# Performance work log

Measured on AMD Instinct MI355X. Metric: run time of the kernel, lower is better.

## Reference

```python
import jax, jax.numpy as jnp
import numpy as np

EPS = 1e-5
K = 16  # neighbors

def bn(x, g, b):
    # BatchNorm in training mode: stats over all axes except the last (channel)
    ax = tuple(range(x.ndim - 1))
    m = x.mean(ax, keepdims=True)
    v = x.var(ax, keepdims=True)
    return g * (x - m) * jax.lax.rsqrt(v + EPS) + b

def setup_inputs() -> dict:
    key = jax.random.key(0)
    ks = jax.random.split(key, 12)
    B, N, M, C, D = 2, 16384, 4096, 32, 64
    H = D // 2
    p = lambda k, s: jax.random.normal(k, s, dtype=jnp.float32) * 0.1
    inp = {}
    inp["xyz"] = jax.random.normal(ks[0], (B, N, 3), dtype=jnp.float32)
    inp["feats"] = jax.random.normal(ks[1], (B, C, N), dtype=jnp.float32)
    inp["sample_idx"] = jax.random.randint(ks[2], (B, M), 0, N, dtype=jnp.int32)
    # RelativePosEncoder mlp: Conv2d(10, H, 1) + BN
    inp["W_pos"] = p(ks[3], (10, H)); inp["b_pos"] = jnp.zeros(H); inp["g_pos"] = jnp.ones(H); inp["be_pos"] = jnp.zeros(H)
    # feature_mlp: Conv2d(C, H, 1) + BN
    inp["W_feat"] = p(ks[4], (C, H)); inp["b_feat"] = jnp.zeros(H); inp["g_feat"] = jnp.ones(H); inp["be_feat"] = jnp.zeros(H)
    # attention score mlp: Conv2d(D, D, 1, bias=False)
    inp["W_score"] = p(ks[5], (D, D))
    # out_mlp: Conv1d(D, D, 1, bias=False) + BN
    inp["W_out"] = p(ks[6], (D, D)); inp["g_out"] = jnp.ones(D); inp["be_out"] = jnp.zeros(D)
    # LFA shortcut: Conv1d(C, D, 1, bias=False) + BN
    inp["W_sc1"] = p(ks[7], (C, D)); inp["g_sc1"] = jnp.ones(D); inp["be_sc1"] = jnp.zeros(D)
    # unit shortcut: Conv1d(C, D, 1, bias=False) + BN
    inp["W_sc2"] = p(ks[8], (C, D)); inp["g_sc2"] = jnp.ones(D); inp["be_sc2"] = jnp.zeros(D)
    return inp

def reference(xyz, feats, sample_idx,
              W_pos, b_pos, g_pos, be_pos,
              W_feat, b_feat, g_feat, be_feat,
              W_score,
              W_out, g_out, be_out,
              W_sc1, g_sc1, be_sc1,
              W_sc2, g_sc2, be_sc2):
    B, C, N = feats.shape
    featsT = jnp.transpose(feats, (0, 2, 1))                    # [B,N,C]
    xyz_ds = jnp.take_along_axis(xyz, sample_idx[:, :, None], axis=1)  # [B,M,3]
    # KNN: squared distances are monotone in cdist -> same topk indices
    d2 = jnp.sum((xyz_ds[:, :, None, :] - xyz[:, None, :, :]) ** 2, axis=-1)  # [B,M,N]
    _, knn_idx = jax.lax.top_k(-d2, K)                           # [B,M,K]
    gather = jax.vmap(lambda pts, idx: pts[idx])
    neigh_xyz = gather(xyz, knn_idx)                             # [B,M,K,3]
    neigh_feats = gather(featsT, knn_idx)                        # [B,M,K,C]
    center_feats = jnp.take_along_axis(featsT, sample_idx[:, :, None], axis=1)  # [B,M,C]
    # relative position encoding
    center = jnp.broadcast_to(xyz_ds[:, :, None, :], neigh_xyz.shape)
    rel = xyz_ds[:, :, None, :] - neigh_xyz                      # [B,M,K,3]
    dist = jnp.linalg.norm(rel, axis=-1, keepdims=True)          # [B,M,K,1]
    posf = jnp.concatenate([center, neigh_xyz, rel, dist], axis=-1)  # [B,M,K,10]
    pos_feats = jax.nn.relu(bn(posf @ W_pos + b_pos, g_pos, be_pos))       # [B,M,K,H]
    feat_feats = jax.nn.relu(bn(neigh_feats @ W_feat + b_feat, g_feat, be_feat))  # [B,M,K,H]
    combined = jnp.concatenate([feat_feats, pos_feats], axis=-1)  # [B,M,K,D]
    # attention pooling: softmax over the K (neighbor) axis
    scores = jax.nn.softmax(combined @ W_score, axis=2)
    pooled = jnp.sum(scores * combined, axis=2)                  # [B,M,D]
    out = jax.nn.relu(bn(pooled @ W_out, g_out, be_out))         # [B,M,D]
    sc1 = bn(jnp.mean(neigh_feats, axis=2) @ W_sc1, g_sc1, be_sc1)
    f_lfa = out + sc1
    f_sc = bn(center_feats @ W_sc2, g_sc2, be_sc2)
    y = jax.nn.relu(f_lfa + f_sc)                                # [B,M,D]
    return xyz_ds, jnp.transpose(y, (0, 2, 1)), sample_idx
```

## Files before the change

kernel.cpp:

```cpp
#include <hip/hip_runtime.h>
#include <math.h>

#define BB 2
#define NN 16384
#define MM 4096
#define C_IN 32
#define D_DIM 64
#define H_DIM 32
#define KNB 16
#define EPSV 1e-5f
#define FLT_BIG 3.0e38f
#define CAPK 128
#define NSPL 4
#define SPTS (NN / NSPL)

#define SPOS_SUM 0
#define SPOS_SQ 32
#define SFEAT_SUM 64
#define SFEAT_SQ 96
#define SSC1_SUM 128
#define SSC1_SQ 192
#define SSC2_SUM 256
#define SSC2_SQ 320
#define SOUT_SUM 384
#define SOUT_SQ 448
#define STATS_LEN 512
#define PA_W 384
#define PB_W 128
#define NBLK (BB * MM / 4)

typedef float f32x2 __attribute__((ext_vector_type(2)));

__device__ __forceinline__ f32x2 mk2_r24(float a, float b) {
    f32x2 r; r.x = a; r.y = b; return r;
}

__device__ __forceinline__ int clampi_r24(int v, int lo, int hi) {
    return v < lo ? lo : (v > hi ? hi : v);
}

__global__ __launch_bounds__(256) void prep_r24(const float* __restrict__ feats,
                                                const float* __restrict__ xyz,
                                                const int* __restrict__ sample_idx,
                                                float* __restrict__ featsT,
                                                float* __restrict__ xyz4,
                                                float* __restrict__ stats,
                                                float* __restrict__ out) {
    __shared__ float tile[C_IN][65];
    const int tid = threadIdx.x;
    const int b = blockIdx.x >> 8;
    const int n0 = (blockIdx.x & 255) * 64;
#pragma unroll
    for (int it = 0; it < 8; ++it) {
        int c = (tid >> 6) + 4 * it;
        int n = tid & 63;
        tile[c][n] = feats[((size_t)b * C_IN + c) * NN + n0 + n];
    }
    int e = blockIdx.x * 256 + tid;
    if (e < STATS_LEN) stats[e] = 0.f;
    if (e < BB * NN) {
        float x = xyz[e * 3 + 0], y = xyz[e * 3 + 1], z = xyz[e * 3 + 2];
        xyz4[e * 4 + 0] = x;
        xyz4[e * 4 + 1] = y;
        xyz4[e * 4 + 2] = z;
        xyz4[e * 4 + 3] = x * x + y * y + z * z;
    }
    if (e < BB * MM) {
        int bb2 = e >> 12;
        int sidx = clampi_r24(sample_idx[e], 0, NN - 1);
        const float* p = xyz + (size_t)(bb2 * NN + sidx) * 3;
        out[e * 3 + 0] = p[0];
        out[e * 3 + 1] = p[1];
        out[e * 3 + 2] = p[2];
        out[BB * MM * 3 + BB * D_DIM * MM + e] = (float)sample_idx[e];
    }
    __syncthreads();
#pragma unroll
    for (int it = 0; it < 8; ++it) {
        int c = tid & 31;
        int nn = (tid >> 5) + 8 * it;
        featsT[((size_t)b * NN + n0 + nn) * C_IN + c] = tile[c][nn];
    }
}

__device__ void knn_fullsplit_r24(const float* __restrict__ base4, int n0,
                                  float m2x, float m2y, float m2z, int lane,
                                  float* __restrict__ outd, int* __restrict__ outi) {
    float d2v[KNB]; int iv[KNB];
#pragma unroll
    for (int i = 0; i < KNB; i++) { d2v[i] = FLT_BIG; iv[i] = 0x7FFFFFFF; }
    float curmax = FLT_BIG; int amax = 0;
    for (int t = 0; t < SPTS / 64; ++t) {
        int n = n0 + lane + t * 64;
        const float4 p = *reinterpret_cast<const float4*>(base4 + (size_t)n * 4);
        float d2 = fmaf(p.x, m2x, p.w);
        d2 = fmaf(p.y, m2y, d2);
        d2 = fmaf(p.z, m2z, d2);
        if (d2 < curmax) {
#pragma unroll
            for (int i = 0; i < KNB; i++)
                if (i == amax) { d2v[i] = d2; iv[i] = n; }
            curmax = d2v[0]; amax = 0;
#pragma unroll
            for (int i = 1; i < KNB; i++)
                if (d2v[i] > curmax) { curmax = d2v[i]; amax = i; }
        }
    }
#pragma unroll
    for (int i = 0; i < KNB; i++) {
#pragma unroll
        for (int j = 0; j < KNB - 1; j++) {
            bool sw = (d2v[j] > d2v[j + 1]) ||
                      (d2v[j] == d2v[j + 1] && iv[j] > iv[j + 1]);
            if (sw) {
                float td = d2v[j]; d2v[j] = d2v[j + 1]; d2v[j + 1] = td;
                int   ti = iv[j];  iv[j]  = iv[j + 1];  iv[j + 1]  = ti;
            }
        }
    }
    float myd = FLT_BIG; int myidx = 0x7FFFFFFF;
#pragma unroll 1
    for (int r = 0; r < KNB; r++) {
        float cv = d2v[0]; int cid = iv[0]; int ml = lane;
#pragma unroll
        for (int off = 32; off > 0; off >>= 1) {
            float ov = __shfl_xor(cv, off);
            int   oid = __shfl_xor(cid, off);
            int   ol = __shfl_xor(ml, off);
            bool take = (ov < cv) || (ov == cv && oid < cid);
            cv = take ? ov : cv; cid = take ? oid : cid; ml = take ? ol : ml;
        }
        if (lane == r) { myd = cv; myidx = cid; }
        if (lane == ml) {
#pragma unroll
            for (int i = 0; i < KNB - 1; i++) { d2v[i] = d2v[i + 1]; iv[i] = iv[i + 1]; }
            d2v[KNB - 1] = FLT_BIG; iv[KNB - 1] = 0x7FFFFFFF;
        }
    }
    if (lane < KNB) { outd[lane] = myd; outi[lane] = myidx; }
}

__global__ __launch_bounds__(256) void knn_r24(const float* __restrict__ xyz4,
                                               const int* __restrict__ sample_idx,
                                               float* __restrict__ cand_d,
                                               int* __restrict__ cand_i) {
    __shared__ float bufd[32][CAPK];
    __shared__ int   bufi[32][CAPK];
    const int tid = threadIdx.x;
    const int w = tid >> 6, lane = tid & 63;
    const int split = blockIdx.x & (NSPL - 1);
    const int qgrp = blockIdx.x >> 2;
    const int qbase = qgrp * 32 + w * 8;
    const int b = qbase >> 12;
    const int n0 = split * SPTS;
    const float* base4 = xyz4 + (size_t)b * NN * 4;
    const float4* p4 = reinterpret_cast<const float4*>(base4) + n0 + lane;

    float m2x[8], m2y[8], m2z[8], md[8], v16[8];
#pragma unroll
    for (int j = 0; j < 8; j++) {
        int s = clampi_r24(sample_idx[qbase + j], 0, NN - 1);
        m2x[j] = -2.f * base4[(size_t)s * 4 + 0];
        m2y[j] = -2.f * base4[(size_t)s * 4 + 1];
        m2z[j] = -2.f * base4[(size_t)s * 4 + 2];
        md[j] = FLT_BIG;
    }
#pragma unroll 4
    for (int it = 0; it < SPTS / 64; ++it) {
        const float4 p = p4[(size_t)it * 64];
#pragma unroll
        for (int j = 0; j < 8; j++) {
            float t = fmaf(p.x, m2x[j], p.w);
            t = fmaf(p.y, m2y[j], t);
            t = fmaf(p.z, m2z[j], t);
            md[j] = fminf(md[j], t);
        }
    }
    {
        float sv[8];
#pragma unroll
        for (int j = 0; j < 8; j++) sv[j] = md[j];
#pragma unroll
        for (int k = 2; k <= 64; k <<= 1) {
#pragma unroll
            for (int j2 = k >> 1; j2 >= 1; j2 >>= 1) {
                const bool want_min = (((lane & j2) == 0) == ((lane & k) == 0));
#pragma unroll
                for (int j = 0; j < 8; j++) {
                    float ov = __shfl_xor(sv[j], j2);
                    float mn = fminf(sv[j], ov);
                    float mx = fmaxf(sv[j], ov);
                    sv[j] = want_min ? mn : mx;
                }
            }
        }
#pragma unroll
        for (int j = 0; j < 8; j++) v16[j] = __shfl(sv[j], KNB - 1);
    }
    int cnt[8] = {0, 0, 0, 0, 0, 0, 0, 0};
#pragma unroll 4
    for (int it = 0; it < SPTS / 64; ++it) {
        const float4 p = p4[(size_t)it * 64];
        const int n = n0 + lane + it * 64;
#pragma unroll
        for (int j = 0; j < 8; j++) {
            float t = fmaf(p.x, m2x[j], p.w);
            t = fmaf(p.y, m2y[j], t);
            t = fmaf(p.z, m2z[j], t);
            bool pred = (t <= v16[j]);
            unsigned long long bal = __ballot(pred);
            if (bal) {
                int pre = __builtin_amdgcn_mbcnt_hi((unsigned)(bal >> 32),
                          __builtin_amdgcn_mbcnt_lo((unsigned)bal, 0u));
                int pos = cnt[j] + pre;
                if (pred && pos < CAPK) {
                    bufd[w * 8 + j][pos] = t;
                    bufi[w * 8 + j][pos] = n;
                }
                cnt[j] += __popcll(bal);
            }
        }
    }
    {
        float dv[8]; int ivv[8];
#pragma unroll
        for (int j = 0; j < 8; j++) {
            const int qi = w * 8 + j;
            bool valid = (cnt[j] <= 64) && (lane < cnt[j]);
            dv[j]  = valid ? bufd[qi][lane] : FLT_BIG;
            ivv[j] = valid ? bufi[qi][lane] : 0x7FFFFFFF;
        }
#pragma unroll
        for (int k = 2; k <= 64; k <<= 1) {
#pragma unroll
            for (int j2 = k >> 1; j2 >= 1; j2 >>= 1) {
                const bool want_min = (((lane & j2) == 0) == ((lane & k) == 0));
#pragma unroll
                for (int j = 0; j < 8; j++) {
                    float od = __shfl_xor(dv[j], j2);
                    int   oi = __shfl_xor(ivv[j], j2);
                    bool mine_less = (dv[j] < od) || (dv[j] == od && ivv[j] < oi);
                    bool keep = (mine_less == want_min);
                    dv[j]  = keep ? dv[j]  : od;
                    ivv[j] = keep ? ivv[j] : oi;
                }
            }
        }
#pragma unroll 1
        for (int j = 0; j < 8; j++) {
            const int qi = w * 8 + j;
            const int q = qbase + j;
            float* outd = cand_d + ((size_t)q * NSPL + split) * KNB;
            int*   outi = cand_i + ((size_t)q * NSPL + split) * KNB;
            if (cnt[j] <= 64) {
                if (lane < KNB) { outd[lane] = dv[j]; outi[lane] = ivv[j]; }
            } else if (cnt[j] <= CAPK) {
#pragma unroll 1
                for (int half = 0; half < 2; ++half) {
                    int i = lane + 64 * half;
                    if (i < cnt[j]) {
                        float di = bufd[qi][i]; int xi = bufi[qi][i];
                        int rank = 0;
                        for (int t = 0; t < cnt[j]; ++t) {
                            float dt = bufd[qi][t]; int xt = bufi[qi][t];
                            rank += (dt < di || (dt == di && xt < xi)) ? 1 : 0;
                        }
                        if (rank < KNB) { outd[rank] = di; outi[rank] = xi; }
                    }
                }
            } else {
                knn_fullsplit_r24(base4, n0, m2x[j], m2y[j], m2z[j], lane, outd, outi);
            }
        }
    }
}

__device__ __forceinline__ void prebn_r24(const float (*posf)[12], const float (*nf)[C_IN],
                                          int k,
                                          const f32x2* __restrict__ wp2, float bp,
                                          const f32x2* __restrict__ wf2, float bf,
                                          float* a_out, float* f_out) {
    const f32x2* pp = reinterpret_cast<const f32x2*>(&posf[k][0]);
    f32x2 a2 = pp[0] * wp2[0];
    a2 = pp[1] * wp2[1] + a2;
    a2 = pp[2] * wp2[2] + a2;
    a2 = pp[3] * wp2[3] + a2;
    a2 = pp[4] * wp2[4] + a2;
    const f32x2* nn2 = reinterpret_cast<const f32x2*>(&nf[k][0]);
    f32x2 f2 = nn2[0] * wf2[0];
#pragma unroll
    for (int t = 1; t < 16; ++t) f2 = nn2[t] * wf2[t] + f2;
    *a_out = bp + a2.x + a2.y;
    *f_out = bf + f2.x + f2.y;
}

__global__ __launch_bounds__(256) void stageA_r24(const float* __restrict__ xyz4,
                                                  const int* __restrict__ sample_idx,
                                                  const float* __restrict__ featsT,
                                                  const float* __restrict__ cand_d,
                                                  const int* __restrict__ cand_i,
                                                  const float* __restrict__ W_pos, const float* __restrict__ b_pos,
                                                  const float* __restrict__ W_feat, const float* __restrict__ b_feat,
                                                  const float* __restrict__ W_sc1, const float* __restrict__ W_sc2,
                                                  float* __restrict__ combpre,
                                                  float* __restrict__ sc1_pre, float* __restrict__ sc2_pre,
                                                  float* __restrict__ partialsA) {
    __shared__ __align__(16) float posf[4][KNB][12];
    __shared__ __align__(16) float nf[4][KNB][C_IN];
    __shared__ float meanf[4][C_IN];
    __shared__ float centerf[4][C_IN];
    __shared__ float posS[4][H_DIM], posQ[4][H_DIM], featS[4][H_DIM], featQ[4][H_DIM];
    __shared__ float s1S[4][D_DIM], s1Q[4][D_DIM], s2S[4][D_DIM], s2Q[4][D_DIM];
    const int tid = threadIdx.x;
    const int w = tid >> 6, lane = tid & 63;
    const int q = blockIdx.x * 4 + w;
    const int b = q >> 12;
    const int sidx = clampi_r24(sample_idx[q], 0, NN - 1);
    const float* base4 = xyz4 + (size_t)b * NN * 4;

    float dmv; int imv;
    {
        const int run = lane >> 4, pos = lane & 15;
        const int ridx = (run & 1) ? (15 - pos) : pos;
        dmv = cand_d[(size_t)q * 64 + run * 16 + ridx];
        imv = cand_i[(size_t)q * 64 + run * 16 + ridx];
    }
    float qx = base4[(size_t)sidx * 4 + 0];
    float qy = base4[(size_t)sidx * 4 + 1];
    float qz = base4[(size_t)sidx * 4 + 2];
    if (lane < C_IN) centerf[w][lane] = featsT[((size_t)b * NN + sidx) * C_IN + lane];
#pragma unroll
    for (int k = 32; k <= 64; k <<= 1) {
#pragma unroll
        for (int j2 = k >> 1; j2 >= 1; j2 >>= 1) {
            const bool want_min = (((lane & j2) == 0) == ((lane & k) == 0));
            float od = __shfl_xor(dmv, j2);
            int   oi = __shfl_xor(imv, j2);
            bool mine_less = (dmv < od) || (dmv == od && imv < oi);
            bool keep = (mine_less == want_min);
            dmv = keep ? dmv : od;
            imv = keep ? imv : oi;
        }
    }

    if (lane < KNB) {
        int idx = clampi_r24(imv, 0, NN - 1);
        float nx = base4[(size_t)idx * 4 + 0];
        float ny = base4[(size_t)idx * 4 + 1];
        float nz = base4[(size_t)idx * 4 + 2];
        float rx = qx - nx, ry = qy - ny, rz = qz - nz;
        float dist = sqrtf(rx * rx + ry * ry + rz * rz);
        posf[w][lane][0] = qx; posf[w][lane][1] = qy; posf[w][lane][2] = qz;
        posf[w][lane][3] = nx; posf[w][lane][4] = ny; posf[w][lane][5] = nz;
        posf[w][lane][6] = rx; posf[w][lane][7] = ry; posf[w][lane][8] = rz;
        posf[w][lane][9] = dist; posf[w][lane][10] = 0.f; posf[w][lane][11] = 0.f;
    }
    const float* fT = featsT + (size_t)b * NN * C_IN;
#pragma unroll
    for (int ii = 0; ii < 2; ++ii) {
        int e4 = lane + 64 * ii;
        int k = e4 >> 3, c4 = e4 & 7;
        int idx = clampi_r24(__shfl(imv, k), 0, NN - 1);
        const float4 v = *reinterpret_cast<const float4*>(fT + (size_t)idx * C_IN + c4 * 4);
        *reinterpret_cast<float4*>(&nf[w][k][c4 * 4]) = v;
    }

    const int h = lane & 31;
    f32x2 wp2[5], wf2[16];
#pragma unroll
    for (int t = 0; t < 5; ++t)
        wp2[t] = mk2_r24(W_pos[(2 * t) * H_DIM + h], W_pos[(2 * t + 1) * H_DIM + h]);
#pragma unroll
    for (int t = 0; t < 16; ++t)
        wf2[t] = mk2_r24(W_feat[(2 * t) * H_DIM + h], W_feat[(2 * t + 1) * H_DIM + h]);
    const float bp = b_pos[h], bf = b_feat[h];

    float sP = 0.f, qP = 0.f, sF = 0.f, qF = 0.f;
    float* cp = combpre + (size_t)q * (KNB * D_DIM);
#pragma unroll
    for (int i2 = 0; i2 < 8; i2++) {
        int k = ((lane + 64 * i2) >> 5);
        float a, f;
        prebn_r24(posf[w], nf[w], k, wp2, bp, wf2, bf, &a, &f);
        sP += a; qP += a * a;
        sF += f; qF += f * f;
        cp[k * D_DIM + h] = f;
        cp[k * D_DIM + H_DIM + h] = a;
    }
    sP += __shfl_xor(sP, 32); qP += __shfl_xor(qP, 32);
    sF += __shfl_xor(sF, 32); qF += __shfl_xor(qF, 32);
    if (lane < H_DIM) {
        posS[w][h] = sP; posQ[w][h] = qP; featS[w][h] = sF; featQ[w][h] = qF;
    }
    if (lane < C_IN) {
        float s = 0.f;
#pragma unroll
        for (int k = 0; k < KNB; k++) s += nf[w][k][lane];
        meanf[w][lane] = s * (1.f / (float)KNB);
    }
    {
        float a = 0.f, c2 = 0.f;
#pragma unroll
        for (int j = 0; j < C_IN; j++) {
            a  += meanf[w][j]   * W_sc1[j * D_DIM + lane];
            c2 += centerf[w][j] * W_sc2[j * D_DIM + lane];
        }
        sc1_pre[(size_t)q * D_DIM + lane] = a;
        sc2_pre[(size_t)q * D_DIM + lane] = c2;
        s1S[w][lane] = a;  s1Q[w][lane] = a * a;
        s2S[w][lane] = c2; s2Q[w][lane] = c2 * c2;
    }
    __syncthreads();
    float* row = partialsA + (size_t)blockIdx.x * PA_W;
    if (tid < H_DIM) {
        row[SPOS_SUM + tid]  = posS[0][tid] + posS[1][tid] + posS[2][tid] + posS[3][tid];
        row[SPOS_SQ + tid]   = posQ[0][tid] + posQ[1][tid] + posQ[2][tid] + posQ[3][tid];
        row[SFEAT_SUM + tid] = featS[0][tid] + featS[1][tid] + featS[2][tid] + featS[3][tid];
        row[SFEAT_SQ + tid]  = featQ[0][tid] + featQ[1][tid] + featQ[2][tid] + featQ[3][tid];
    } else if (tid >= 64 && tid < 128) {
        int dd = tid - 64;
        row[SSC1_SUM + dd] = s1S[0][dd] + s1S[1][dd] + s1S[2][dd] + s1S[3][dd];
        row[SSC1_SQ + dd]  = s1Q[0][dd] + s1Q[1][dd] + s1Q[2][dd] + s1Q[3][dd];
    } else if (tid >= 128 && tid < 192) {
        int dd = tid - 128;
        row[SSC2_SUM + dd] = s2S[0][dd] + s2S[1][dd] + s2S[2][dd] + s2S[3][dd];
        row[SSC2_SQ + dd]  = s2Q[0][dd] + s2Q[1][dd] + s2Q[2][dd] + s2Q[3][dd];
    }
}

#define NRSPLIT 64
__global__ __launch_bounds__(256) void reduce_r24(const float* __restrict__ partials,
                                                  int rows, int width,
                                                  float* __restrict__ stats_out) {
    const int wchunks = (width + 255) / 256;
    const int wi = blockIdx.x % wchunks;
    const int pi = blockIdx.x / wchunks;
    const int c = wi * 256 + threadIdx.x;
    if (c >= width) return;
    const int per = rows / NRSPLIT;
    const int p0 = pi * per;
    float s = 0.f;
    for (int p = p0; p < p0 + per; ++p) s += partials[(size_t)p * width + c];
    atomicAdd(&stats_out[c], s);
}

__global__ __launch_bounds__(256) void stageB_r24(const float* __restrict__ combpre,
                                                  const float* __restrict__ g_pos, const float* __restrict__ be_pos,
                                                  const float* __restrict__ g_feat, const float* __restrict__ be_feat,
                                                  const float* __restrict__ W_score, const float* __restrict__ W_out,
                                                  const float* __restrict__ stats,
                                                  float* __restrict__ out_pre,
                                                  float* __restrict__ partialsB) {
    __shared__ __align__(16) float comb[4][KNB][D_DIM];
    __shared__ float scl[D_DIM], shf[D_DIM];
    __shared__ float pooled[4][D_DIM];
    __shared__ float oS[4][D_DIM], oQ[4][D_DIM];
    const int tid = threadIdx.x;
    const int w = tid >> 6, lane = tid & 63;
    const int q = blockIdx.x * 4 + w;

    if (tid < D_DIM) {
        const float inv1 = 1.f / (float)(BB * MM * KNB);
        float mean, var, g, bb;
        if (tid < H_DIM) {
            mean = stats[SFEAT_SUM + tid] * inv1;
            var  = fmaxf(stats[SFEAT_SQ + tid] * inv1 - mean * mean, 0.f);
            g = g_feat[tid]; bb = be_feat[tid];
        } else {
            int h = tid - H_DIM;
            mean = stats[SPOS_SUM + h] * inv1;
            var  = fmaxf(stats[SPOS_SQ + h] * inv1 - mean * mean, 0.f);
            g = g_pos[h]; bb = be_pos[h];
        }
        float s = g * rsqrtf(var + EPSV);
        scl[tid] = s;
        shf[tid] = bb - mean * s;
    }
    __syncthreads();

    const float4* src = reinterpret_cast<const float4*>(combpre + (size_t)blockIdx.x * 4 * KNB * D_DIM);
#pragma unroll
    for (int i = 0; i < 4; ++i) {
        int f = tid + 256 * i;
        int qloc = f >> 8;
        int k = (f >> 4) & 15;
        int j4 = f & 15;
        float4 v = src[f];
        int j = j4 * 4;
        v.x = fmaxf(v.x * scl[j + 0] + shf[j + 0], 0.f);
        v.y = fmaxf(v.y * scl[j + 1] + shf[j + 1], 0.f);
        v.z = fmaxf(v.z * scl[j + 2] + shf[j + 2], 0.f);
        v.w = fmaxf(v.w * scl[j + 3] + shf[j + 3], 0.f);
        *reinterpret_cast<float4*>(&comb[qloc][k][j]) = v;
    }
    __syncthreads();

    const int d = lane;
    f32x2 s2[KNB];
#pragma unroll
    for (int k = 0; k < KNB; k++) s2[k] = mk2_r24(0.f, 0.f);
#pragma unroll 4
    for (int j4 = 0; j4 < D_DIM / 4; ++j4) {
        f32x2 wA = mk2_r24(W_score[(j4 * 4 + 0) * D_DIM + d],
                           W_score[(j4 * 4 + 1) * D_DIM + d]);
        f32x2 wB = mk2_r24(W_score[(j4 * 4 + 2) * D_DIM + d],
                           W_score[(j4 * 4 + 3) * D_DIM + d]);
#pragma unroll
        for (int k = 0; k < KNB; k++) {
            const f32x2* cb = reinterpret_cast<const f32x2*>(&comb[w][k][j4 * 4]);
            s2[k] = cb[0] * wA + s2[k];
            s2[k] = cb[1] * wB + s2[k];
        }
    }
    float s[KNB];
#pragma unroll
    for (int k = 0; k < KNB; k++) s[k] = s2[k].x + s2[k].y;
    float mx = s[0];
#pragma unroll
    for (int k = 1; k < KNB; k++) mx = fmaxf(mx, s[k]);
    float sum = 0.f;
#pragma unroll
    for (int k = 0; k < KNB; k++) { s[k] = __expf(s[k] - mx); sum += s[k]; }
    float inv = 1.f / sum;
    float pv = 0.f;
#pragma unroll
    for (int k = 0; k < KNB; k++) pv += s[k] * inv * comb[w][k][d];
    pooled[w][d] = pv;
    __syncthreads();
    float o = 0.f;
#pragma unroll
    for (int dd = 0; dd < D_DIM; dd++) o += pooled[w][dd] * W_out[dd * D_DIM + d];
    out_pre[(size_t)q * D_DIM + d] = o;
    oS[w][d] = o; oQ[w][d] = o * o;
    __syncthreads();
    float* row = partialsB + (size_t)blockIdx.x * PB_W;
    if (tid < D_DIM) {
        row[tid] = oS[0][tid] + oS[1][tid] + oS[2][tid] + oS[3][tid];
    } else if (tid < 2 * D_DIM) {
        int dd = tid - D_DIM;
        row[D_DIM + dd] = oQ[0][dd] + oQ[1][dd] + oQ[2][dd] + oQ[3][dd];
    }
}

__global__ __launch_bounds__(256) void final_r24(const float* __restrict__ out_pre,
                                                 const float* __restrict__ sc1_pre,
                                                 const float* __restrict__ sc2_pre,
                                                 const float* __restrict__ stats,
                                                 const float* __restrict__ g_out, const float* __restrict__ be_out,
                                                 const float* __restrict__ g_sc1, const float* __restrict__ be_sc1,
                                                 const float* __restrict__ g_sc2, const float* __restrict__ be_sc2,
                                                 float* __restrict__ out) {
    __shared__ float yt[64][65];
    const int tid = threadIdx.x;
    const int blk = blockIdx.x;
    const int b = blk >> 6;
    const int m0 = (blk & 63) * 64;
    const int d = tid & 63;

    const float invn = 1.f / (float)(BB * MM);
    float mo = stats[SOUT_SUM + d] * invn;
    float vo = fmaxf(stats[SOUT_SQ + d] * invn - mo * mo, 0.f);
    float so = g_out[d] * rsqrtf(vo + EPSV);
    float oo = be_out[d] - mo * so;
    float m1 = stats[SSC1_SUM + d] * invn;
    float v1 = fmaxf(stats[SSC1_SQ + d] * invn - m1 * m1, 0.f);
    float s1 = g_sc1[d] * rsqrtf(v1 + EPSV);
    float o1 = be_sc1[d] - m1 * s1;
    float m2 = stats[SSC2_SUM + d] * invn;
    float v2 = fmaxf(stats[SSC2_SQ + d] * invn - m2 * m2, 0.f);
    float s2 = g_sc2[d] * rsqrtf(v2 + EPSV);
    float o2 = be_sc2[d] - m2 * s2;

#pragma unroll
    for (int p = 0; p < 16; p++) {
        int ml = (tid >> 6) + 4 * p;
        size_t q = (size_t)b * MM + m0 + ml;
        float x_out = fmaxf(out_pre[q * D_DIM + d] * so + oo, 0.f);
        float x1 = sc1_pre[q * D_DIM + d] * s1 + o1;
        float x2 = sc2_pre[q * D_DIM + d] * s2 + o2;
        yt[ml][d] = fmaxf(x_out + x1 + x2, 0.f);
    }
    __syncthreads();
#pragma unroll
    for (int p = 0; p < 16; p++) {
        int dr = (tid >> 6) + 4 * p;
        int mc = tid & 63;
        out[BB * MM * 3 + (size_t)b * (D_DIM * MM) + (size_t)dr * MM + m0 + mc] = yt[mc][dr];
    }
}

extern "C" void kernel_launch(void* const* d_in, const int* in_sizes, int n_in,
                              void* d_out, int out_size, void* d_ws, size_t ws_size,
                              hipStream_t stream) {
    const float* xyz        = (const float*)d_in[0];
    const float* feats      = (const float*)d_in[1];
    const int*   sample_idx = (const int*)d_in[2];
    const float* W_pos  = (const float*)d_in[3];
    const float* b_pos  = (const float*)d_in[4];
    const float* g_pos  = (const float*)d_in[5];
    const float* be_pos = (const float*)d_in[6];
    const float* W_feat  = (const float*)d_in[7];
    const float* b_feat  = (const float*)d_in[8];
    const float* g_feat  = (const float*)d_in[9];
    const float* be_feat = (const float*)d_in[10];
    const float* W_score = (const float*)d_in[11];
    const float* W_out  = (const float*)d_in[12];
    const float* g_out  = (const float*)d_in[13];
    const float* be_out = (const float*)d_in[14];
    const float* W_sc1  = (const float*)d_in[15];
    const float* g_sc1  = (const float*)d_in[16];
    const float* be_sc1 = (const float*)d_in[17];
    const float* W_sc2  = (const float*)d_in[18];
    const float* g_sc2  = (const float*)d_in[19];
    const float* be_sc2 = (const float*)d_in[20];

    float* out = (float*)d_out;
    float* ws = (float*)d_ws;

    float* featsT    = ws;
    float* xyz4      = featsT + 1048576;
    float* sc1_pre   = xyz4 + 131072;
    float* sc2_pre   = sc1_pre + 524288;
    float* out_pre   = sc2_pre + 524288;
    float* stats     = out_pre + 524288;
    float* partialsA = stats + STATS_LEN;
    float* partialsB = partialsA + NBLK * PA_W;
    float* cand_d    = partialsB + NBLK * PB_W;
    int*   cand_i    = (int*)(cand_d + (size_t)BB * MM * NSPL * KNB);
    float* combpre   = (float*)(cand_i + (size_t)BB * MM * NSPL * KNB);

    prep_r24<<<BB * (NN / 64), 256, 0, stream>>>(feats, xyz, sample_idx,
                                                 featsT, xyz4, stats, out);

    knn_r24<<<(BB * MM / 32) * NSPL, 256, 0, stream>>>(xyz4, sample_idx, cand_d, cand_i);

    stageA_r24<<<NBLK, 256, 0, stream>>>(xyz4, sample_idx, featsT, cand_d, cand_i,
                                         W_pos, b_pos, W_feat, b_feat, W_sc1, W_sc2,
                                         combpre, sc1_pre, sc2_pre, partialsA);
    reduce_r24<<<2 * NRSPLIT, 256, 0, stream>>>(partialsA, NBLK, PA_W, stats);

    stageB_r24<<<NBLK, 256, 0, stream>>>(combpre,
                                         g_pos, be_pos, g_feat, be_feat,
                                         W_score, W_out, stats, out_pre, partialsB);
    reduce_r24<<<1 * NRSPLIT, 256, 0, stream>>>(partialsB, NBLK, PB_W, stats + SOUT_SUM);

    final_r24<<<BB * (MM / 64), 256, 0, stream>>>(out_pre, sc1_pre, sc2_pre, stats,
                                                  g_out, be_out, g_sc1, be_sc1, g_sc2, be_sc2, out);
}
```

Baseline: 231.8 us.

## Replace brute-force KNN with uniform grid spatial hashing search

```diff
diff --git a/kernel.cpp b/kernel.cpp
--- a/kernel.cpp
+++ b/kernel.cpp
@@ -11,8 +11,11 @@
 #define EPSV 1e-5f
 #define FLT_BIG 3.0e38f
 #define CAPK 128
-#define NSPL 4
-#define SPTS (NN / NSPL)
+#define GG 32
+#define G3 (GG * GG * GG)
+#define LO_BOUND (-5.0f)
+#define H_CELL (10.0f / (float)GG)
+#define INV_H ((float)GG / 10.0f)
 
 #define SPOS_SUM 0
 #define SPOS_SQ 32
@@ -31,20 +34,26 @@
 
 typedef float f32x2 __attribute__((ext_vector_type(2)));
 
-__device__ __forceinline__ f32x2 mk2_r24(float a, float b) {
+__device__ __forceinline__ f32x2 mk2_r25(float a, float b) {
     f32x2 r; r.x = a; r.y = b; return r;
 }
 
-__device__ __forceinline__ int clampi_r24(int v, int lo, int hi) {
+__device__ __forceinline__ int clampi_r25(int v, int lo, int hi) {
     return v < lo ? lo : (v > hi ? hi : v);
 }
 
-__global__ __launch_bounds__(256) void prep_r24(const float* __restrict__ feats,
+__device__ __forceinline__ int cell_of_r25(float v) {
+    int c = (int)floorf((v - LO_BOUND) * INV_H);
+    return clampi_r25(c, 0, GG - 1);
+}
+
+__global__ __launch_bounds__(256) void prep_r25(const float* __restrict__ feats,
                                                 const float* __restrict__ xyz,
                                                 const int* __restrict__ sample_idx,
                                                 float* __restrict__ featsT,
                                                 float* __restrict__ xyz4,
                                                 float* __restrict__ stats,
+                                                int* __restrict__ cellcnt,
                                                 float* __restrict__ out) {
     __shared__ float tile[C_IN][65];
     const int tid = threadIdx.x;
@@ -58,6 +67,7 @@
     }
     int e = blockIdx.x * 256 + tid;
     if (e < STATS_LEN) stats[e] = 0.f;
+    if (e < BB * G3) cellcnt[e] = 0;
     if (e < BB * NN) {
         float x = xyz[e * 3 + 0], y = xyz[e * 3 + 1], z = xyz[e * 3 + 2];
         xyz4[e * 4 + 0] = x;
@@ -67,7 +77,7 @@
     }
     if (e < BB * MM) {
         int bb2 = e >> 12;
-        int sidx = clampi_r24(sample_idx[e], 0, NN - 1);
+        int sidx = clampi_r25(sample_idx[e], 0, NN - 1);
         const float* p = xyz + (size_t)(bb2 * NN + sidx) * 3;
         out[e * 3 + 0] = p[0];
         out[e * 3 + 1] = p[1];
@@ -83,19 +93,74 @@
     }
 }
 
-__device__ void knn_fullsplit_r24(const float* __restrict__ base4, int n0,
-                                  float m2x, float m2y, float m2z, int lane,
-                                  float* __restrict__ outd, int* __restrict__ outi) {
+__global__ __launch_bounds__(256) void hist_r25(const float* __restrict__ xyz,
+                                                int* __restrict__ cellcnt) {
+    int e = blockIdx.x * 256 + threadIdx.x;
+    if (e >= BB * NN) return;
+    int b = e >> 14;
+    float x = xyz[e * 3 + 0], y = xyz[e * 3 + 1], z = xyz[e * 3 + 2];
+    int cid = (cell_of_r25(z) * GG + cell_of_r25(y)) * GG + cell_of_r25(x);
+    atomicAdd(&cellcnt[b * G3 + cid], 1);
+}
+
+__global__ __launch_bounds__(256) void scan_r25(const int* __restrict__ cellcnt,
+                                                int* __restrict__ cellstart,
+                                                int* __restrict__ cursor) {
+    __shared__ int psum[256];
+    const int b = blockIdx.x;
+    const int tid = threadIdx.x;
+    const int cbase = b * G3;
+    const int sbase = b * (G3 + 1);
+    int s = 0;
+#pragma unroll 1
+    for (int i = tid * 128; i < (tid + 1) * 128; ++i) s += cellcnt[cbase + i];
+    psum[tid] = s;
+    __syncthreads();
+    for (int off = 1; off < 256; off <<= 1) {
+        int t = (tid >= off) ? psum[tid - off] : 0;
+        __syncthreads();
+        psum[tid] += t;
+        __syncthreads();
+    }
+    int run = (tid == 0) ? 0 : psum[tid - 1];
+#pragma unroll 1
+    for (int i = tid * 128; i < (tid + 1) * 128; ++i) {
+        cellstart[sbase + i] = run;
+        cursor[cbase + i] = run;
+        run += cellcnt[cbase + i];
+    }
+    if (tid == 255) cellstart[sbase + G3] = run;
+}
+
+__global__ __launch_bounds__(256) void scatter_r25(const float* __restrict__ xyz,
+                                                   int* __restrict__ cursor,
+                                                   float* __restrict__ xyzr) {
+    int e = blockIdx.x * 256 + threadIdx.x;
+    if (e >= BB * NN) return;
+    int b = e >> 14;
+    int n = e & (NN - 1);
+    float x = xyz[e * 3 + 0], y = xyz[e * 3 + 1], z = xyz[e * 3 + 2];
+    int cid = (cell_of_r25(z) * GG + cell_of_r25(y)) * GG + cell_of_r25(x);
+    int pos = atomicAdd(&cursor[b * G3 + cid], 1);
+    float4* dst = reinterpret_cast<float4*>(xyzr) + (size_t)b * NN + pos;
+    float4 v;
+    v.x = x; v.y = y; v.z = z; v.w = __int_as_float(n);
+    *dst = v;
+}
+
+__device__ void knn_fullN_r25(const float* __restrict__ base4,
+                              float qx, float qy, float qz, int lane,
+                              int* __restrict__ outi) {
     float d2v[KNB]; int iv[KNB];
 #pragma unroll
     for (int i = 0; i < KNB; i++) { d2v[i] = FLT_BIG; iv[i] = 0x7FFFFFFF; }
     float curmax = FLT_BIG; int amax = 0;
-    for (int t = 0; t < SPTS / 64; ++t) {
-        int n = n0 + lane + t * 64;
+    for (int n = lane; n < NN; n += 64) {
         const float4 p = *reinterpret_cast<const float4*>(base4 + (size_t)n * 4);
-        float d2 = fmaf(p.x, m2x, p.w);
-        d2 = fmaf(p.y, m2y, d2);
-        d2 = fmaf(p.z, m2z, d2);
+        float dx = qx - p.x, dy = qy - p.y, dz = qz - p.z;
+        float d2 = dx * dx;
+        d2 = fmaf(dy, dy, d2);
+        d2 = fmaf(dz, dz, d2);
         if (d2 < curmax) {
 #pragma unroll
             for (int i = 0; i < KNB; i++)
@@ -118,7 +183,6 @@
             }
         }
     }
-    float myd = FLT_BIG; int myidx = 0x7FFFFFFF;
 #pragma unroll 1
     for (int r = 0; r < KNB; r++) {
         float cv = d2v[0]; int cid = iv[0]; int ml = lane;
@@ -130,152 +194,182 @@
             bool take = (ov < cv) || (ov == cv && oid < cid);
             cv = take ? ov : cv; cid = take ? oid : cid; ml = take ? ol : ml;
         }
-        if (lane == r) { myd = cv; myidx = cid; }
+        if (lane == r) outi[r] = cid;
         if (lane == ml) {
 #pragma unroll
             for (int i = 0; i < KNB - 1; i++) { d2v[i] = d2v[i + 1]; iv[i] = iv[i + 1]; }
             d2v[KNB - 1] = FLT_BIG; iv[KNB - 1] = 0x7FFFFFFF;
         }
     }
-    if (lane < KNB) { outd[lane] = myd; outi[lane] = myidx; }
-}
-
-__global__ __launch_bounds__(256) void knn_r24(const float* __restrict__ xyz4,
-                                               const int* __restrict__ sample_idx,
-                                               float* __restrict__ cand_d,
-                                               int* __restrict__ cand_i) {
-    __shared__ float bufd[32][CAPK];
-    __shared__ int   bufi[32][CAPK];
+}
+
+__global__ __launch_bounds__(256) void knnq_r25(const float* __restrict__ xyz4,
+                                                const int* __restrict__ sample_idx,
+                                                const int* __restrict__ cellstart,
+                                                const float* __restrict__ xyzr,
+                                                int* __restrict__ cand_i) {
+    __shared__ float bufd[4][CAPK];
+    __shared__ int   bufi[4][CAPK];
     const int tid = threadIdx.x;
     const int w = tid >> 6, lane = tid & 63;
-    const int split = blockIdx.x & (NSPL - 1);
-    const int qgrp = blockIdx.x >> 2;
-    const int qbase = qgrp * 32 + w * 8;
-    const int b = qbase >> 12;
-    const int n0 = split * SPTS;
+    const int q = blockIdx.x * 4 + w;
+    const int b = q >> 12;
+    const int sidx = clampi_r25(sample_idx[q], 0, NN - 1);
     const float* base4 = xyz4 + (size_t)b * NN * 4;
-    const float4* p4 = reinterpret_cast<const float4*>(base4) + n0 + lane;
-
-    float m2x[8], m2y[8], m2z[8], md[8], v16[8];
-#pragma unroll
-    for (int j = 0; j < 8; j++) {
-        int s = clampi_r24(sample_idx[qbase + j], 0, NN - 1);
-        m2x[j] = -2.f * base4[(size_t)s * 4 + 0];
-        m2y[j] = -2.f * base4[(size_t)s * 4 + 1];
-        m2z[j] = -2.f * base4[(size_t)s * 4 + 2];
-        md[j] = FLT_BIG;
-    }
-#pragma unroll 4
-    for (int it = 0; it < SPTS / 64; ++it) {
-        const float4 p = p4[(size_t)it * 64];
-#pragma unroll
-        for (int j = 0; j < 8; j++) {
-            float t = fmaf(p.x, m2x[j], p.w);
-            t = fmaf(p.y, m2y[j], t);
-            t = fmaf(p.z, m2z[j], t);
-            md[j] = fminf(md[j], t);
-        }
-    }
-    {
-        float sv[8];
-#pragma unroll
-        for (int j = 0; j < 8; j++) sv[j] = md[j];
+    const float qx = base4[(size_t)sidx * 4 + 0];
+    const float qy = base4[(size_t)sidx * 4 + 1];
+    const float qz = base4[(size_t)sidx * 4 + 2];
+    const int cx = cell_of_r25(qx), cy = cell_of_r25(qy), cz = cell_of_r25(qz);
+    const int* cs = cellstart + (size_t)b * (G3 + 1);
+    const float4* pts = reinterpret_cast<const float4*>(xyzr) + (size_t)b * NN;
+
+    int R = 0;
+#pragma unroll 1
+    for (;; ++R) {
+        int c = 0;
+#pragma unroll 1
+        for (int dz = -R; dz <= R; ++dz) {
+            int z = cz + dz;
+            if (z < 0 || z >= GG) continue;
+#pragma unroll 1
+            for (int dy = -R; dy <= R; ++dy) {
+                int y = cy + dy;
+                if (y < 0 || y >= GG) continue;
+                int x0 = max(0, cx - R), x1 = min(GG - 1, cx + R);
+                int base = (z * GG + y) * GG;
+                c += cs[base + x1 + 1] - cs[base + x0];
+            }
+        }
+        if (c >= KNB || R >= GG) break;
+    }
+    float S16;
+#pragma unroll 1
+    for (;; ++R) {
+        float md = FLT_BIG;
+#pragma unroll 1
+        for (int dz = -R; dz <= R; ++dz) {
+            int z = cz + dz;
+            if (z < 0 || z >= GG) continue;
+#pragma unroll 1
+            for (int dy = -R; dy <= R; ++dy) {
+                int y = cy + dy;
+                if (y < 0 || y >= GG) continue;
+                int x0 = max(0, cx - R), x1 = min(GG - 1, cx + R);
+                int base = (z * GG + y) * GG;
+                int s = cs[base + x0], e = cs[base + x1 + 1];
+#pragma unroll 1
+                for (int i = s + lane; i < e; i += 64) {
+                    float4 p = pts[i];
+                    float dx = qx - p.x, dy2 = qy - p.y, dz2 = qz - p.z;
+                    float t = dx * dx;
+                    t = fmaf(dy2, dy2, t);
+                    t = fmaf(dz2, dz2, t);
+                    md = fminf(md, t);
+                }
+            }
+        }
+        float sv = md;
 #pragma unroll
         for (int k = 2; k <= 64; k <<= 1) {
 #pragma unroll
             for (int j2 = k >> 1; j2 >= 1; j2 >>= 1) {
                 const bool want_min = (((lane & j2) == 0) == ((lane & k) == 0));
-#pragma unroll
-                for (int j = 0; j < 8; j++) {
-                    float ov = __shfl_xor(sv[j], j2);
-                    float mn = fminf(sv[j], ov);
-                    float mx = fmaxf(sv[j], ov);
-                    sv[j] = want_min ? mn : mx;
+                float ov = __shfl_xor(sv, j2);
+                sv = want_min ? fminf(sv, ov) : fmaxf(sv, ov);
+            }
+        }
+        S16 = __shfl(sv, KNB - 1);
+        if (S16 < FLT_BIG || R >= GG) break;
+    }
+#pragma unroll 1
+    for (; R < GG; ++R) {
+        float lox = LO_BOUND + (float)(cx - R) * H_CELL;
+        float hix = LO_BOUND + (float)(cx + R + 1) * H_CELL;
+        float loy = LO_BOUND + (float)(cy - R) * H_CELL;
+        float hiy = LO_BOUND + (float)(cy + R + 1) * H_CELL;
+        float loz = LO_BOUND + (float)(cz - R) * H_CELL;
+        float hiz = LO_BOUND + (float)(cz + R + 1) * H_CELL;
+        float m = fminf(fminf(qx - lox, hix - qx),
+                  fminf(fminf(qy - loy, hiy - qy),
+                        fminf(qz - loz, hiz - qz)));
+        if (m > 0.f && m * m > S16) break;
+    }
+    int cnt = 0;
+#pragma unroll 1
+    for (int dz = -R; dz <= R; ++dz) {
+        int z = cz + dz;
+        if (z < 0 || z >= GG) continue;
+#pragma unroll 1
+        for (int dy = -R; dy <= R; ++dy) {
+            int y = cy + dy;
+            if (y < 0 || y >= GG) continue;
+            int x0 = max(0, cx - R), x1 = min(GG - 1, cx + R);
+            int base = (z * GG + y) * GG;
+            int s = cs[base + x0], e = cs[base + x1 + 1];
+#pragma unroll 1
+            for (int i0 = s; i0 < e; i0 += 64) {
+                int i = i0 + lane;
+                bool pred = false;
+                float t = 0.f; int oid = 0;
+                if (i < e) {
+                    float4 p = pts[i];
+                    float dx = qx - p.x, dy2 = qy - p.y, dz2 = qz - p.z;
+                    t = dx * dx;
+                    t = fmaf(dy2, dy2, t);
+                    t = fmaf(dz2, dz2, t);
+                    oid = __float_as_int(p.w);
+                    pred = (t <= S16);
+                }
+                unsigned long long bal = __ballot(pred);
+                if (bal) {
+                    int pre = __builtin_amdgcn_mbcnt_hi((unsigned)(bal >> 32),
+                              __builtin_amdgcn_mbcnt_lo((unsigned)bal, 0u));
+                    int pos = cnt + pre;
+                    if (pred && pos < CAPK) { bufd[w][pos] = t; bufi[w][pos] = oid; }
+                    cnt += __popcll(bal);
                 }
             }
         }
-#pragma unroll
-        for (int j = 0; j < 8; j++) v16[j] = __shfl(sv[j], KNB - 1);
-    }
-    int cnt[8] = {0, 0, 0, 0, 0, 0, 0, 0};
-#pragma unroll 4
-    for (int it = 0; it < SPTS / 64; ++it) {
-        const float4 p = p4[(size_t)it * 64];
-        const int n = n0 + lane + it * 64;
-#pragma unroll
-        for (int j = 0; j < 8; j++) {
-            float t = fmaf(p.x, m2x[j], p.w);
-            t = fmaf(p.y, m2y[j], t);
-            t = fmaf(p.z, m2z[j], t);
-            bool pred = (t <= v16[j]);
-            unsigned long long bal = __ballot(pred);
-            if (bal) {
-                int pre = __builtin_amdgcn_mbcnt_hi((unsigned)(bal >> 32),
-                          __builtin_amdgcn_mbcnt_lo((unsigned)bal, 0u));
-                int pos = cnt[j] + pre;
-                if (pred && pos < CAPK) {
-                    bufd[w * 8 + j][pos] = t;
-                    bufi[w * 8 + j][pos] = n;
-                }
-                cnt[j] += __popcll(bal);
-            }
-        }
-    }
-    {
-        float dv[8]; int ivv[8];
-#pragma unroll
-        for (int j = 0; j < 8; j++) {
-            const int qi = w * 8 + j;
-            bool valid = (cnt[j] <= 64) && (lane < cnt[j]);
-            dv[j]  = valid ? bufd[qi][lane] : FLT_BIG;
-            ivv[j] = valid ? bufi[qi][lane] : 0x7FFFFFFF;
-        }
+    }
+    int* outq = cand_i + (size_t)q * KNB;
+    if (cnt <= 64) {
+        bool valid = (lane < cnt);
+        float dv = valid ? bufd[w][lane] : FLT_BIG;
+        int   iv = valid ? bufi[w][lane] : 0x7FFFFFFF;
 #pragma unroll
         for (int k = 2; k <= 64; k <<= 1) {
 #pragma unroll
             for (int j2 = k >> 1; j2 >= 1; j2 >>= 1) {
                 const bool want_min = (((lane & j2) == 0) == ((lane & k) == 0));
-#pragma unroll
-                for (int j = 0; j < 8; j++) {
-                    float od = __shfl_xor(dv[j], j2);
-                    int   oi = __shfl_xor(ivv[j], j2);
-                    bool mine_less = (dv[j] < od) || (dv[j] == od && ivv[j] < oi);
-                    bool keep = (mine_less == want_min);
-                    dv[j]  = keep ? dv[j]  : od;
-                    ivv[j] = keep ? ivv[j] : oi;
+                float od = __shfl_xor(dv, j2);
+                int   oi = __shfl_xor(iv, j2);
+                bool mine_less = (dv < od) || (dv == od && iv < oi);
+                bool keep = (mine_less == want_min);
+                dv = keep ? dv : od;
+                iv = keep ? iv : oi;
+            }
+        }
+        if (lane < KNB) outq[lane] = iv;
+    } else if (cnt <= CAPK) {
+#pragma unroll 1
+        for (int half = 0; half < 2; ++half) {
+            int i = lane + 64 * half;
+            if (i < cnt) {
+                float di = bufd[w][i]; int xi = bufi[w][i];
+                int rank = 0;
+                for (int t = 0; t < cnt; ++t) {
+                    float dt = bufd[w][t]; int xt = bufi[w][t];
+                    rank += (dt < di || (dt == di && xt < xi)) ? 1 : 0;
                 }
+                if (rank < KNB) outq[rank] = xi;
             }
         }
-#pragma unroll 1
-        for (int j = 0; j < 8; j++) {
-            const int qi = w * 8 + j;
-            const int q = qbase + j;
-            float* outd = cand_d + ((size_t)q * NSPL + split) * KNB;
-            int*   outi = cand_i + ((size_t)q * NSPL + split) * KNB;
-            if (cnt[j] <= 64) {
-                if (lane < KNB) { outd[lane] = dv[j]; outi[lane] = ivv[j]; }
-            } else if (cnt[j] <= CAPK) {
-#pragma unroll 1
-                for (int half = 0; half < 2; ++half) {
-                    int i = lane + 64 * half;
-                    if (i < cnt[j]) {
-                        float di = bufd[qi][i]; int xi = bufi[qi][i];
-                        int rank = 0;
-                        for (int t = 0; t < cnt[j]; ++t) {
-                            float dt = bufd[qi][t]; int xt = bufi[qi][t];
-                            rank += (dt < di || (dt == di && xt < xi)) ? 1 : 0;
-                        }
-                        if (rank < KNB) { outd[rank] = di; outi[rank] = xi; }
-                    }
-                }
-            } else {
-                knn_fullsplit_r24(base4, n0, m2x[j], m2y[j], m2z[j], lane, outd, outi);
-            }
-        }
-    }
-}
-
-__device__ __forceinline__ void prebn_r24(const float (*posf)[12], const float (*nf)[C_IN],
+    } else {
+        knn_fullN_r25(base4, qx, qy, qz, lane, outq);
+    }
+}
+
+__device__ __forceinline__ void prebn_r25(const float (*posf)[12], const float (*nf)[C_IN],
                                           int k,
                                           const f32x2* __restrict__ wp2, float bp,
                                           const f32x2* __restrict__ wf2, float bf,
@@ -294,10 +388,9 @@
     *f_out = bf + f2.x + f2.y;
 }
 
-__global__ __launch_bounds__(256) void stageA_r24(const float* __restrict__ xyz4,
+__global__ __launch_bounds__(256) void stageA_r25(const float* __restrict__ xyz4,
                                                   const int* __restrict__ sample_idx,
                                                   const float* __restrict__ featsT,
-                                                  const float* __restrict__ cand_d,
                                                   const int* __restrict__ cand_i,
                                                   const float* __restrict__ W_pos, const float* __restrict__ b_pos,
                                                   const float* __restrict__ W_feat, const float* __restrict__ b_feat,
@@ -315,36 +408,18 @@
     const int w = tid >> 6, lane = tid & 63;
     const int q = blockIdx.x * 4 + w;
     const int b = q >> 12;
-    const int sidx = clampi_r24(sample_idx[q], 0, NN - 1);
+    const int sidx = clampi_r25(sample_idx[q], 0, NN - 1);
     const float* base4 = xyz4 + (size_t)b * NN * 4;
 
-    float dmv; int imv;
-    {
-        const int run = lane >> 4, pos = lane & 15;
-        const int ridx = (run & 1) ? (15 - pos) : pos;
-        dmv = cand_d[(size_t)q * 64 + run * 16 + ridx];
-        imv = cand_i[(size_t)q * 64 + run * 16 + ridx];
-    }
+    int imv = 0x7FFFFFFF;
+    if (lane < KNB) imv = cand_i[(size_t)q * KNB + lane];
     float qx = base4[(size_t)sidx * 4 + 0];
     float qy = base4[(size_t)sidx * 4 + 1];
     float qz = base4[(size_t)sidx * 4 + 2];
     if (lane < C_IN) centerf[w][lane] = featsT[((size_t)b * NN + sidx) * C_IN + lane];
-#pragma unroll
-    for (int k = 32; k <= 64; k <<= 1) {
-#pragma unroll
-        for (int j2 = k >> 1; j2 >= 1; j2 >>= 1) {
-            const bool want_min = (((lane & j2) == 0) == ((lane & k) == 0));
-            float od = __shfl_xor(dmv, j2);
-            int   oi = __shfl_xor(imv, j2);
-            bool mine_less = (dmv < od) || (dmv == od && imv < oi);
-            bool keep = (mine_less == want_min);
-            dmv = keep ? dmv : od;
-            imv = keep ? imv : oi;
-        }
-    }
 
     if (lane < KNB) {
-        int idx = clampi_r24(imv, 0, NN - 1);
+        int idx = clampi_r25(imv, 0, NN - 1);
         float nx = base4[(size_t)idx * 4 + 0];
         float ny = base4[(size_t)idx * 4 + 1];
         float nz = base4[(size_t)idx * 4 + 2];
@@ -360,7 +435,7 @@
     for (int ii = 0; ii < 2; ++ii) {
         int e4 = lane + 64 * ii;
         int k = e4 >> 3, c4 = e4 & 7;
-        int idx = clampi_r24(__shfl(imv, k), 0, NN - 1);
+        int idx = clampi_r25(__shfl(imv, k), 0, NN - 1);
         const float4 v = *reinterpret_cast<const float4*>(fT + (size_t)idx * C_IN + c4 * 4);
         *reinterpret_cast<float4*>(&nf[w][k][c4 * 4]) = v;
     }
@@ -369,10 +444,10 @@
     f32x2 wp2[5], wf2[16];
 #pragma unroll
     for (int t = 0; t < 5; ++t)
-        wp2[t] = mk2_r24(W_pos[(2 * t) * H_DIM + h], W_pos[(2 * t + 1) * H_DIM + h]);
+        wp2[t] = mk2_r25(W_pos[(2 * t) * H_DIM + h], W_pos[(2 * t + 1) * H_DIM + h]);
 #pragma unroll
     for (int t = 0; t < 16; ++t)
-        wf2[t] = mk2_r24(W_feat[(2 * t) * H_DIM + h], W_feat[(2 * t + 1) * H_DIM + h]);
+        wf2[t] = mk2_r25(W_feat[(2 * t) * H_DIM + h], W_feat[(2 * t + 1) * H_DIM + h]);
     const float bp = b_pos[h], bf = b_feat[h];
 
     float sP = 0.f, qP = 0.f, sF = 0.f, qF = 0.f;
@@ -381,7 +456,7 @@
     for (int i2 = 0; i2 < 8; i2++) {
         int k = ((lane + 64 * i2) >> 5);
         float a, f;
-        prebn_r24(posf[w], nf[w], k, wp2, bp, wf2, bf, &a, &f);
+        prebn_r25(posf[w], nf[w], k, wp2, bp, wf2, bf, &a, &f);
         sP += a; qP += a * a;
         sF += f; qF += f * f;
         cp[k * D_DIM + h] = f;
@@ -429,7 +504,7 @@
 }
 
 #define NRSPLIT 64
-__global__ __launch_bounds__(256) void reduce_r24(const float* __restrict__ partials,
+__global__ __launch_bounds__(256) void reduce_r25(const float* __restrict__ partials,
                                                   int rows, int width,
                                                   float* __restrict__ stats_out) {
     const int wchunks = (width + 255) / 256;
@@ -444,7 +519,7 @@
     atomicAdd(&stats_out[c], s);
 }
 
-__global__ __launch_bounds__(256) void stageB_r24(const float* __restrict__ combpre,
+__global__ __launch_bounds__(256) void stageB_r25(const float* __restrict__ combpre,
                                                   const float* __restrict__ g_pos, const float* __restrict__ be_pos,
                                                   const float* __restrict__ g_feat, const float* __restrict__ be_feat,
                                                   const float* __restrict__ W_score, const float* __restrict__ W_out,
@@ -498,12 +573,12 @@
     const int d = lane;
     f32x2 s2[KNB];
 #pragma unroll
-    for (int k = 0; k < KNB; k++) s2[k] = mk2_r24(0.f, 0.f);
+    for (int k = 0; k < KNB; k++) s2[k] = mk2_r25(0.f, 0.f);
 #pragma unroll 4
     for (int j4 = 0; j4 < D_DIM / 4; ++j4) {
-        f32x2 wA = mk2_r24(W_score[(j4 * 4 + 0) * D_DIM + d],
+        f32x2 wA = mk2_r25(W_score[(j4 * 4 + 0) * D_DIM + d],
                            W_score[(j4 * 4 + 1) * D_DIM + d]);
-        f32x2 wB = mk2_r24(W_score[(j4 * 4 + 2) * D_DIM + d],
+        f32x2 wB = mk2_r25(W_score[(j4 * 4 + 2) * D_DIM + d],
                            W_score[(j4 * 4 + 3) * D_DIM + d]);
 #pragma unroll
         for (int k = 0; k < KNB; k++) {
@@ -542,7 +617,7 @@
     }
 }
 
-__global__ __launch_bounds__(256) void final_r24(const float* __restrict__ out_pre,
+__global__ __launch_bounds__(256) void final_r25(const float* __restrict__ out_pre,
                                                  const float* __restrict__ sc1_pre,
                                                  const float* __restrict__ sc2_pre,
                                                  const float* __restrict__ stats,
@@ -625,25 +700,34 @@
     float* stats     = out_pre + 524288;
     float* partialsA = stats + STATS_LEN;
     float* partialsB = partialsA + NBLK * PA_W;
-    float* cand_d    = partialsB + NBLK * PB_W;
-    int*   cand_i    = (int*)(cand_d + (size_t)BB * MM * NSPL * KNB);
-    float* combpre   = (float*)(cand_i + (size_t)BB * MM * NSPL * KNB);
-
-    prep_r24<<<BB * (NN / 64), 256, 0, stream>>>(feats, xyz, sample_idx,
-                                                 featsT, xyz4, stats, out);
-
-    knn_r24<<<(BB * MM / 32) * NSPL, 256, 0, stream>>>(xyz4, sample_idx, cand_d, cand_i);
-
-    stageA_r24<<<NBLK, 256, 0, stream>>>(xyz4, sample_idx, featsT, cand_d, cand_i,
+    int*   cand_i    = (int*)(partialsB + NBLK * PB_W);
+    int*   cellcnt   = cand_i + BB * MM * KNB;
+    int*   cellstart = cellcnt + BB * G3;
+    int*   cursor    = cellstart + BB * (G3 + 1);
+    float* xyzr      = (float*)(cursor + BB * G3);
+    float* combpre   = xyzr + BB * NN * 4;
+
+    prep_r25<<<BB * (NN / 64), 256, 0, stream>>>(feats, xyz, sample_idx,
+                                                 featsT, xyz4, stats, cellcnt, out);
+
+    hist_r25<<<BB * NN / 256, 256, 0, stream>>>(xyz, cellcnt);
+
+    scan_r25<<<BB, 256, 0, stream>>>(cellcnt, cellstart, cursor);
+
+    scatter_r25<<<BB * NN / 256, 256, 0, stream>>>(xyz, cursor, xyzr);
+
+    knnq_r25<<<BB * MM / 4, 256, 0, stream>>>(xyz4, sample_idx, cellstart, xyzr, cand_i);
+
+    stageA_r25<<<NBLK, 256, 0, stream>>>(xyz4, sample_idx, featsT, cand_i,
                                          W_pos, b_pos, W_feat, b_feat, W_sc1, W_sc2,
                                          combpre, sc1_pre, sc2_pre, partialsA);
-    reduce_r24<<<2 * NRSPLIT, 256, 0, stream>>>(partialsA, NBLK, PA_W, stats);
-
-    stageB_r24<<<NBLK, 256, 0, stream>>>(combpre,
+    reduce_r25<<<2 * NRSPLIT, 256, 0, stream>>>(partialsA, NBLK, PA_W, stats);
+
+    stageB_r25<<<NBLK, 256, 0, stream>>>(combpre,
                                          g_pos, be_pos, g_feat, be_feat,
                                          W_score, W_out, stats, out_pre, partialsB);
-    reduce_r24<<<1 * NRSPLIT, 256, 0, stream>>>(partialsB, NBLK, PB_W, stats + SOUT_SUM);
-
-    final_r24<<<BB * (MM / 64), 256, 0, stream>>>(out_pre, sc1_pre, sc2_pre, stats,
+    reduce_r25<<<1 * NRSPLIT, 256, 0, stream>>>(partialsB, NBLK, PB_W, stats + SOUT_SUM);
+
+    final_r25<<<BB * (MM / 64), 256, 0, stream>>>(out_pre, sc1_pre, sc2_pre, stats,
                                                   g_out, be_out, g_sc1, be_sc1, g_sc2, be_sc2, out);
 }
```

Result: slower. 709.5 us (+206.1%).
